# Kernel tuning notes

Measured on AMD Instinct MI355X. Metric: run time of the kernel, lower is better.

Reference implementation:

```python
import jax, jax.numpy as jnp
import numpy as np

EPS_BN = 1e-5
K_INTERP = 8
K_NEIGH = 16


def _bn(x, g, b):
    # BatchNorm1d in training mode: batch stats over rows (biased var), eps=1e-5
    m = x.mean(axis=0)
    v = x.var(axis=0)
    return (x - m) * jax.lax.rsqrt(v + EPS_BN) * g + b


def _dist(a, b):
    # a:(B,N,3), b:(B,M,3) -> Euclidean distance (B,N,M), computed via the
    # quadratic expansion (clamped at 0) instead of materializing (B,N,M,3)
    d2 = (jnp.sum(a * a, -1)[:, :, None] + jnp.sum(b * b, -1)[:, None, :]
          - 2.0 * jnp.einsum('bnc,bmc->bnm', a, b))
    return jnp.sqrt(jnp.maximum(d2, 0.0))


def _gather(feats, idx):
    # feats:(B,M,C), idx:(B,N,K) int -> (B,N,K,C)
    return jax.vmap(lambda f, i: f[i])(feats, idx)


def setup_inputs() -> dict:
    key = jax.random.key(0)
    B, N1, N2, DS, DD, DOUT = 4, 4096, 1024, 128, 64, 256
    ks = jax.random.split(key, 20)
    s = 0.02
    inp = {
        'p1': jax.random.uniform(ks[0], (B * N1, 3), jnp.float32),
        'x1': jax.random.normal(ks[1], (B * N1, DD), jnp.float32),
        'o1': (jnp.arange(B, dtype=jnp.int32) + 1) * N1,
        'p2': jax.random.uniform(ks[2], (B * N2, 3), jnp.float32),
        'x2': jax.random.normal(ks[3], (B * N2, DS), jnp.float32),
        'o2': (jnp.arange(B, dtype=jnp.int32) + 1) * N2,
        'batch_size': B,
        # dense_mlp: Linear(DD,DS) + BN
        'W_dense': jax.random.normal(ks[4], (DD, DS), jnp.float32) * s,
        'b_dense': jnp.zeros((DS,), jnp.float32),
        'g_dense': jnp.ones((DS,), jnp.float32),
        'bt_dense': jnp.zeros((DS,), jnp.float32),
        # CrossAttentionPointTransformerLayer (dim=DS, hidden_mult=1)
        'Wq': jax.random.normal(ks[5], (DS, DS), jnp.float32) * s,
        'Wk': jax.random.normal(ks[6], (DS, DS), jnp.float32) * s,
        'Wv': jax.random.normal(ks[7], (DS, DS), jnp.float32) * s,
        'W1': jax.random.normal(ks[8], (DS, DS), jnp.float32) * s,
        'b1': jnp.zeros((DS,), jnp.float32),
        'g1': jnp.ones((DS,), jnp.float32),
        'bt1': jnp.zeros((DS,), jnp.float32),
        'W2': jax.random.normal(ks[9], (DS, DS), jnp.float32) * s,
        'b2': jnp.zeros((DS,), jnp.float32),
        # output mlp: Linear(DS+DD, DOUT) + BN
        'W_out': jax.random.normal(ks[10], (DS + DD, DOUT), jnp.float32) * s,
        'b_out': jnp.zeros((DOUT,), jnp.float32),
        'g_out': jnp.ones((DOUT,), jnp.float32),
        'bt_out': jnp.zeros((DOUT,), jnp.float32),
    }
    return inp


def reference(p1, x1, o1, p2, x2, o2, batch_size,
              W_dense, b_dense, g_dense, bt_dense,
              Wq, Wk, Wv, W1, b1, g1, bt1, W2, b2,
              W_out, b_out, g_out, bt_out):
    B = int(batch_size)
    N1 = p1.shape[0] // B
    N2 = p2.shape[0] // B
    DS = x2.shape[-1]

    # dense_mlp
    x1_dense = jax.nn.relu(_bn(x1 @ W_dense + b_dense, g_dense, bt_dense))  # (B*N1, DS)

    # pointops.interpolation(p2, p1, x2, o2, o1, k=8): inverse-distance kNN interp
    p1b = p1.reshape(B, N1, 3)
    p2b = p2.reshape(B, N2, 3)
    x2b = x2.reshape(B, N2, DS)
    d12 = _dist(p1b, p2b)                       # (B,N1,N2)
    negd, idx = jax.lax.top_k(-d12, K_INTERP)   # k nearest in p2
    dknn = -negd
    recip = 1.0 / (dknn + 1e-8)
    w = recip / recip.sum(-1, keepdims=True)    # (B,N1,8)
    x2_interp = jnp.einsum('bnk,bnkc->bnc', w, _gather(x2b, idx))  # (B,N1,DS)

    # CrossAttentionPointTransformerLayer(x_e=x1_dense, x_r=x_d=x2_interp, pos=p1)
    x_e = x1_dense.reshape(B, N1, DS)
    q = x_e @ Wq
    k = x2_interp @ Wk
    v = x2_interp @ Wv
    rel_dist = _dist(p1b, p1b)                  # (B,N1,N1)
    _, nidx = jax.lax.top_k(-rel_dist, K_NEIGH) # 16 nearest neighbors
    kg = _gather(k, nidx)                        # (B,N1,16,DS)
    vg = _gather(v, nidx)
    xeg = _gather(x_e, nidx)
    qk_rel = q[:, :, None, :] - kg
    v2 = vg + xeg
    h = (qk_rel + xeg).reshape(-1, DS)           # (B*N1*16, DS)
    h = jax.nn.relu(_bn(h @ W1 + b1, g1, bt1))
    sim = (h @ W2 + b2).reshape(B, N1, K_NEIGH, DS)
    attn = jax.nn.softmax(sim, axis=-2)          # over neighbors
    agg = jnp.einsum('bnkc,bnkc->bnc', attn, v2).reshape(B * N1, DS)

    # output mlp
    x = jax.nn.relu(_bn(jnp.concatenate([agg, x1], axis=-1) @ W_out + b_out,
                        g_out, bt_out))
    return (p1, x, o1)
```

## Files before the change

### kernel.cpp

```cpp
#include <hip/hip_runtime.h>
#include <math.h>

#define BB 4
#define NN1 4096
#define NN2 1024
#define DS 128
#define DD 64
#define DOUT 256
#define M1 16384
#define MH 262144
#define KCAT 192
#define KI 8
#define KN 16

#define OUT_P1 49152
#define OUT_X  49152
#define OUT_O1 4243456


static const size_t OFF_HPRE = 0;
static const size_t OFF_WTS  = 16777216;
static const size_t OFF_TMP  = 33554432;
static const size_t OFF_XD   = OFF_TMP  + 2097152;
static const size_t OFF_XI   = OFF_XD   + 2097152;
static const size_t OFF_Q    = OFF_XI   + 2097152;
static const size_t OFF_K    = OFF_Q    + 2097152;
static const size_t OFF_V    = OFF_K    + 2097152;
static const size_t OFF_OUTP = OFF_V    + 2097152;
static const size_t OFF_NIDX = OFF_OUTP + 4194304;
static const size_t OFF_STAT = OFF_NIDX + 262144;
static const size_t OFF_P1Q  = OFF_STAT + 4096;
static const size_t OFF_P2Q  = OFF_P1Q  + 65536;
static const size_t OFF_P1S  = OFF_P2Q  + 16384;
static const size_t OFF_P2S  = OFF_P1S  + 65536;

#define WDH 0
#define WDL 8192
#define WQH 16384
#define WQL 32768
#define WKH 49152
#define WKL 65536
#define WVH 81920
#define WVL 98304
#define W1H 114688
#define W1L 131072
#define W2H 147456
#define W2L 163840
#define WOH 180224
#define WOL 229376

typedef __attribute__((ext_vector_type(8))) short short8;
typedef __attribute__((ext_vector_type(4))) float floatx4;
typedef __attribute__((ext_vector_type(2))) float float2v;

__device__ inline unsigned short f2bf(float f) {
    union { float f; unsigned int u; } x; x.f = f;
    unsigned int r = x.u + 0x7fffu + ((x.u >> 16) & 1u);
    return (unsigned short)(r >> 16);
}
__device__ inline float bf2f(unsigned short h) {
    union { unsigned int u; float f; } x; x.u = ((unsigned int)h) << 16;
    return x.f;
}
__device__ inline unsigned long long shfl_xor_u64(unsigned long long v, int m) {
    unsigned lo = (unsigned)v, hi = (unsigned)(v >> 32);
    lo = (unsigned)__shfl_xor((int)lo, m);
    hi = (unsigned)__shfl_xor((int)hi, m);
    return ((unsigned long long)hi << 32) | lo;
}

#define PRO_STAT  (OUT_P1 + BB)
#define PRO_PACK  (PRO_STAT + 3072)
#define PRO_TOTAL (PRO_PACK + M1 + BB*NN2)
#define NPRO 285
struct SwzParams {
    const float* W[7];
    unsigned short* hi[7];
    unsigned short* lo[7];
    int N[7];
    int fid0[8];
};
__global__ __launch_bounds__(256) void k_prolog(
    const float* __restrict__ p1, const int* __restrict__ o1,
    const float* __restrict__ p2, float* __restrict__ out,
    float* __restrict__ stat, float4* __restrict__ p1q,
    float4* __restrict__ p2q, float* __restrict__ p1s,
    float* __restrict__ p2s, SwzParams p)
{
    if (blockIdx.x < NPRO) {
        int i = blockIdx.x * 256 + threadIdx.x;
        if (i < OUT_P1) out[i] = p1[i];
        else if (i < PRO_STAT) out[OUT_O1 + (i - OUT_P1)] = (float)o1[i - OUT_P1];
        else if (i < PRO_PACK) stat[i - PRO_STAT] = 0.f;
        else if (i < PRO_TOTAL) {
            int j = i - PRO_PACK;
            const float* src; float4* dst; float* ps; int jj;
            if (j < M1) { src = p1; dst = p1q; ps = p1s; jj = j; }
            else        { src = p2; dst = p2q; ps = p2s; jj = j - M1; }
            float x = src[jj*3+0] * 16384.f;
            float y = src[jj*3+1] * 16384.f;
            float z = src[jj*3+2] * 16384.f;
            float n = fmaf(z, z, fmaf(y, y, x*x));
            dst[jj] = make_float4(x, y, z, n);
            int pb8 = (jj >> 1)*8 + (jj & 1);
            ps[pb8]   = x; ps[pb8+2] = y;
            ps[pb8+4] = z; ps[pb8+6] = n;
        }
        return;
    }
    int fid = (blockIdx.x - NPRO)*4 + (threadIdx.x >> 6);
    int lane = threadIdx.x & 63;
    if (fid >= 272) return;
    int seg = 0;
    #pragma unroll
    for (int i = 1; i < 7; i++) if (fid >= p.fid0[i]) seg = i;
    int f = fid - p.fid0[seg];
    const float* W = p.W[seg];
    int N = p.N[seg];
    int ncj = N >> 4;
    int slab = f / ncj, cj = f - slab*ncj;
    int n  = cj*16 + (lane & 15);
    int k0 = slab*32 + (lane >> 4)*8;
    unsigned int oh[8], ol[8];
    #pragma unroll
    for (int j = 0; j < 8; j++) {
        float v = W[(size_t)(k0 + j) * N + n];
        unsigned short h = f2bf(v);
        oh[j] = h;
        ol[j] = f2bf(v - bf2f(h));
    }
    uint4 ph, pl;
    ph.x = oh[0] | (oh[1] << 16); ph.y = oh[2] | (oh[3] << 16);
    ph.z = oh[4] | (oh[5] << 16); ph.w = oh[6] | (oh[7] << 16);
    pl.x = ol[0] | (ol[1] << 16); pl.y = ol[2] | (ol[3] << 16);
    pl.z = ol[4] | (ol[5] << 16); pl.w = ol[6] | (ol[7] << 16);
    ((uint4*)p.hi[seg])[f*64 + lane] = ph;
    ((uint4*)p.lo[seg])[f*64 + lane] = pl;
}

template<int N, int K, int MODE, int STATS, int BNA>
__global__ __launch_bounds__(256) void k_gemm_mf(
    const float* __restrict__ Amat, const unsigned short* __restrict__ Whi,
    const unsigned short* __restrict__ Wlo, const float* __restrict__ bias,
    float* __restrict__ C, const float* __restrict__ aux,
    float* __restrict__ sums, float* __restrict__ sumsq,
    const float* __restrict__ bsums, const float* __restrict__ bsumsq,
    const float* __restrict__ bg, const float* __restrict__ bbt)
{
    __shared__ float sstat[STATS ? 2*N : 1];
    __shared__ float sbn[BNA ? 2*DS : 1];
    const int t = threadIdx.x, w = t >> 6, lane = t & 63;
    const int quad = lane >> 4, c = lane & 15;
    const int row = blockIdx.x*64 + w*16 + c;
    const int sA = (MODE == 2) ? DS : K;
    constexpr int nslab = K >> 5;
    constexpr int ncj = N >> 4;
    const int seg = (MODE == 3) ? blockIdx.y : 0;
    const float* Abase = (MODE == 3 && seg > 0) ? aux : Amat;
    const unsigned short* WhiS = Whi + (size_t)seg*32768;
    const unsigned short* WloS = Wlo + (size_t)seg*32768;
    float* CS = C + (size_t)seg*2097152;
    unsigned short* CS16 = (unsigned short*)C + (size_t)seg*4194304;
    if (STATS) {
        for (int i = t; i < 2*N; i += 256) sstat[i] = 0.f;
    }
    if (BNA) {
        if (t < DS) {
            const float invM = 1.f / (float)M1;
            float m   = bsums[t] * invM;
            float var = bsumsq[t] * invM - m*m;
            float sc  = bg[t] * rsqrtf(var + 1e-5f);
            sbn[t] = sc;
            sbn[DS + t] = bbt[t] - m * sc;
        }
    }
    if (STATS || BNA) __syncthreads();

    floatx4 acc[ncj];
    #pragma unroll
    for (int cj = 0; cj < ncj; cj++) acc[cj] = (floatx4){0.f,0.f,0.f,0.f};

    #pragma unroll
    for (int slab = 0; slab < nslab; slab++) {
        const int kk = slab*32 + quad*8;
        const float* src;
        if (MODE == 2 && kk >= DS) src = aux + (size_t)row*DD + (kk - DS);
        else                       src = Abase + (size_t)row*sA + kk;
        floatx4 va = *(const floatx4*)src;
        floatx4 vb = *(const floatx4*)(src + 4);
        if (BNA && MODE == 3 && seg == 0) {
            #pragma unroll
            for (int j = 0; j < 4; j++) {
                va[j] = fmaxf(fmaf(va[j], sbn[kk+j],   sbn[DS+kk+j]),   0.f);
                vb[j] = fmaxf(fmaf(vb[j], sbn[kk+4+j], sbn[DS+kk+4+j]), 0.f);
            }
        }
        short8 ahi, alo;
        #pragma unroll
        for (int j = 0; j < 4; j++) {
            unsigned short h = f2bf(va[j]);
            ahi[j] = (short)h; alo[j] = (short)f2bf(va[j] - bf2f(h));
        }
        #pragma unroll
        for (int j = 0; j < 4; j++) {
            unsigned short h = f2bf(vb[j]);
            ahi[4+j] = (short)h; alo[4+j] = (short)f2bf(vb[j] - bf2f(h));
        }
        const short8* bh = (const short8*)WhiS + (size_t)slab*ncj*64;
        const short8* bl = (const short8*)WloS + (size_t)slab*ncj*64;
        #pragma unroll
        for (int cj = 0; cj < ncj; cj++) {
            short8 bhv = bh[cj*64 + lane];
            short8 blv = bl[cj*64 + lane];
            acc[cj] = __builtin_amdgcn_mfma_f32_16x16x32_bf16(alo, bhv, acc[cj], 0, 0, 0);
            acc[cj] = __builtin_amdgcn_mfma_f32_16x16x32_bf16(ahi, blv, acc[cj], 0, 0, 0);
            acc[cj] = __builtin_amdgcn_mfma_f32_16x16x32_bf16(ahi, bhv, acc[cj], 0, 0, 0);
        }
    }
    const int rbase = blockIdx.x*64 + w*16 + quad*4;
    #pragma unroll
    for (int cj = 0; cj < ncj; cj++) {
        const float bb = bias ? bias[cj*16 + c] : 0.f;
        float s = 0.f, ss = 0.f;
        #pragma unroll
        for (int p = 0; p < 4; p++) {
            float v = acc[cj][p] + bb;
            if (MODE == 3) {
                if (seg > 0) {
                    float xv = Amat[(size_t)(rbase + p)*DS + cj*16 + c];
                    if (BNA) xv = fmaxf(fmaf(xv, sbn[cj*16+c], sbn[DS+cj*16+c]), 0.f);
                    if (seg == 1) v = xv - v;
                    else          v += xv;
                }
                CS16[(size_t)(rbase + p)*N + cj*16 + c] = f2bf(v);
            } else {
                CS[(size_t)(rbase + p)*N + cj*16 + c] = v;
            }
            if (STATS) { s += v; ss += v*v; }
        }
        if (STATS) {
            s  += __shfl_xor(s, 16);  s  += __shfl_xor(s, 32);
            ss += __shfl_xor(ss, 16); ss += __shfl_xor(ss, 32);
            if (quad == 0) {
                atomicAdd(&sstat[cj*16 + c], s);
                atomicAdd(&sstat[N + cj*16 + c], ss);
            }
        }
    }
    if (STATS) {
        __syncthreads();
        for (int i = t; i < N; i += 256) {
            atomicAdd(&sums[i],  sstat[i]);
            atomicAdd(&sumsq[i], sstat[N + i]);
        }
    }
}

__global__ __launch_bounds__(256) void k_gemm_h(
    const unsigned short* __restrict__ q, const unsigned short* __restrict__ e,
    const int* __restrict__ nidx,
    const unsigned short* __restrict__ W1sw, const float* __restrict__ b1,
    unsigned short* __restrict__ hpre,
    float* __restrict__ sums, float* __restrict__ sumsq)
{
    __shared__ unsigned short WF[16384];
    __shared__ unsigned short outT[128*128];
    __shared__ float sstat[256];
    const int t = threadIdx.x;
    const int w = t >> 6, lane = t & 63;
    sstat[t] = 0.f;
    #pragma unroll
    for (int i = 0; i < 8; i++)
        ((uint4*)WF)[t + 256*i] = ((const uint4*)W1sw)[t + 256*i];
    __syncthreads();

    const int quad = lane >> 4, c = lane & 15;
    const int r0 = blockIdx.x * 128 + w * 32;
    const int nid0 = nidx[r0 + c];
    const int nid1 = nidx[r0 + 16 + c];
    const int pr0 = r0 >> 4;
    const int pr1 = pr0 + 1;

    floatx4 acc[2][8];
    #pragma unroll
    for (int ti = 0; ti < 2; ti++)
        #pragma unroll
        for (int cj = 0; cj < 8; cj++)
            acc[ti][cj] = (floatx4){0.f, 0.f, 0.f, 0.f};

    for (int ks = 0; ks < 4; ks++) {
        short8 bf[8];
        #pragma unroll
        for (int cj = 0; cj < 8; cj++)
            bf[cj] = ((const short8*)WF)[(ks*8 + cj)*64 + lane];
        const int ko = ks*32 + quad*8;
        #pragma unroll
        for (int ti = 0; ti < 2; ti++) {
            const int pr = ti ? pr1 : pr0;
            const int m  = ti ? nid1 : nid0;
            uint4 qv = *(const uint4*)(q + (size_t)pr*DS + ko);
            uint4 ev = *(const uint4*)(e + (size_t)m*DS + ko);
            unsigned qw[4] = {qv.x, qv.y, qv.z, qv.w};
            unsigned ew[4] = {ev.x, ev.y, ev.z, ev.w};
            short8 af;
            #pragma unroll
            for (int j = 0; j < 4; j++) {
                float f0 = bf2f((unsigned short)(qw[j] & 0xffffu))
                         + bf2f((unsigned short)(ew[j] & 0xffffu));
                float f1 = bf2f((unsigned short)(qw[j] >> 16))
                         + bf2f((unsigned short)(ew[j] >> 16));
                af[2*j]   = (short)f2bf(f0);
                af[2*j+1] = (short)f2bf(f1);
            }
            #pragma unroll
            for (int cj = 0; cj < 8; cj++)
                acc[ti][cj] = __builtin_amdgcn_mfma_f32_16x16x32_bf16(af, bf[cj], acc[ti][cj], 0, 0, 0);
        }
    }

    #pragma unroll
    for (int cj = 0; cj < 8; cj++) {
        const float bb = b1[cj*16 + c];
        float s = 0.f, ss = 0.f;
        #pragma unroll
        for (int ti = 0; ti < 2; ti++)
            #pragma unroll
            for (int p = 0; p < 4; p++) {
                float v = acc[ti][cj][p] + bb;
                s += v; ss += v*v;
                int lr = w*32 + ti*16 + quad*4 + p;
                outT[lr*128 + cj*16 + c] = f2bf(v);
            }
        s  += __shfl_xor(s, 16);  s  += __shfl_xor(s, 32);
        ss += __shfl_xor(ss, 16); ss += __shfl_xor(ss, 32);
        if (quad == 0) {
            atomicAdd(&sstat[cj*16 + c], s);
            atomicAdd(&sstat[128 + cj*16 + c], ss);
        }
    }
    __syncthreads();
    unsigned short* gdst = hpre + (size_t)blockIdx.x * 128 * 128;
    #pragma unroll
    for (int i = 0; i < 8; i++)
        ((uint4*)gdst)[t + 256*i] = ((const uint4*)outT)[t + 256*i];
    if (t < 128) atomicAdd(&sums[t], sstat[t]);
    else         atomicAdd(&sumsq[t - 128], sstat[t]);
}

__global__ __launch_bounds__(256) void k_attn2(
    const unsigned short* __restrict__ hpre, const float* __restrict__ sums_h,
    const float* __restrict__ sumsq_h, const float* __restrict__ g1,
    const float* __restrict__ bt1, const unsigned short* __restrict__ W2sw,
    const unsigned short* __restrict__ v, const int* __restrict__ nidx,
    float* __restrict__ agg)
{
    __shared__ unsigned short WF[16384];
    __shared__ float s_sc[DS], s_sh[DS];
    const int t = threadIdx.x;
    #pragma unroll
    for (int i = 0; i < 8; i++)
        ((uint4*)WF)[t + 256*i] = ((const uint4*)W2sw)[t + 256*i];
    if (t < DS) {
        const float invM = 1.f / (float)MH;
        float m   = sums_h[t] * invM;
        float var = sumsq_h[t] * invM - m*m;
        float sc  = g1[t] * rsqrtf(var + 1e-5f);
        s_sc[t] = sc;
        s_sh[t] = bt1[t] - m * sc;
    }
    __syncthreads();

    const int w = t >> 6, lane = t & 63;
    const int gp = blockIdx.x * 4 + w;
    const int quad = lane >> 4, c = lane & 15;

    floatx4 acc[8];
    #pragma unroll
    for (int cj = 0; cj < 8; cj++) acc[cj] = (floatx4){0.f, 0.f, 0.f, 0.f};

    for (int ks = 0; ks < 4; ks++) {
        const int ko = ks*32 + quad*8;
        const unsigned short* hp = hpre + ((size_t)gp*16 + c)*DS + ko;
        uint4 hv = *(const uint4*)hp;
        floatx4 sc0 = *(const floatx4*)&s_sc[ko];
        floatx4 sc1 = *(const floatx4*)&s_sc[ko + 4];
        floatx4 sh0 = *(const floatx4*)&s_sh[ko];
        floatx4 sh1 = *(const floatx4*)&s_sh[ko + 4];
        unsigned int hw[4] = {hv.x, hv.y, hv.z, hv.w};
        short8 af;
        #pragma unroll
        for (int j = 0; j < 4; j++) {
            unsigned short u0 = (unsigned short)(hw[j] & 0xffffu);
            unsigned short u1 = (unsigned short)(hw[j] >> 16);
            float f0 = fmaxf(fmaf(bf2f(u0), (j<2)?sc0[2*j]:sc1[2*j-4],   (j<2)?sh0[2*j]:sh1[2*j-4]),   0.f);
            float f1 = fmaxf(fmaf(bf2f(u1), (j<2)?sc0[2*j+1]:sc1[2*j-3], (j<2)?sh0[2*j+1]:sh1[2*j-3]), 0.f);
            af[2*j]   = (short)f2bf(f0);
            af[2*j+1] = (short)f2bf(f1);
        }
        #pragma unroll
        for (int cj = 0; cj < 8; cj++) {
            short8 bfv = ((const short8*)WF)[(ks*8 + cj)*64 + lane];
            acc[cj] = __builtin_amdgcn_mfma_f32_16x16x32_bf16(af, bfv, acc[cj], 0, 0, 0);
        }
    }

    int nid[4];
    #pragma unroll
    for (int p = 0; p < 4; p++) nid[p] = nidx[gp*16 + quad*4 + p];

    #pragma unroll
    for (int cj = 0; cj < 8; cj++) {
        float m4 = fmaxf(fmaxf(acc[cj][0], acc[cj][1]), fmaxf(acc[cj][2], acc[cj][3]));
        m4 = fmaxf(m4, __shfl_xor(m4, 16));
        m4 = fmaxf(m4, __shfl_xor(m4, 32));
        float e[4]; float s4 = 0.f;
        #pragma unroll
        for (int p = 0; p < 4; p++) { e[p] = __expf(acc[cj][p] - m4); s4 += e[p]; }
        s4 += __shfl_xor(s4, 16); s4 += __shfl_xor(s4, 32);
        const float inv = 1.f / s4;
        const int col = cj*16 + c;
        float a = 0.f;
        #pragma unroll
        for (int p = 0; p < 4; p++)
            a = fmaf(e[p]*inv, bf2f(v[(size_t)nid[p]*DS + col]), a);
        a += __shfl_xor(a, 16); a += __shfl_xor(a, 32);
        if (quad == 0) agg[(size_t)gp*DS + col] = a;
    }
}

__global__ __launch_bounds__(256) void k_bnrelu(
    const float4* __restrict__ X, const float* __restrict__ sums,
    const float* __restrict__ sumsq, const float* __restrict__ g,
    const float* __restrict__ bt, float invM,
    float4* __restrict__ Y, size_t total4, int N)
{
    size_t i = (size_t)blockIdx.x * 256 + threadIdx.x;
    if (i < total4) {
        int c = (int)((i*4) & (size_t)(N - 1));
        float4 sm = *(const float4*)(sums + c);
        float4 sq = *(const float4*)(sumsq + c);
        float4 gg = *(const float4*)(g + c);
        float4 bb = *(const float4*)(bt + c);
        float4 x = X[i], y;
        float m0 = sm.x*invM, m1 = sm.y*invM, m2 = sm.z*invM, m3 = sm.w*invM;
        float s0 = gg.x*rsqrtf(sq.x*invM - m0*m0 + 1e-5f);
        float s1 = gg.y*rsqrtf(sq.y*invM - m1*m1 + 1e-5f);
        float s2 = gg.z*rsqrtf(sq.z*invM - m2*m2 + 1e-5f);
        float s3 = gg.w*rsqrtf(sq.w*invM - m3*m3 + 1e-5f);
        y.x = fmaxf(fmaf(x.x, s0, bb.x - m0*s0), 0.f);
        y.y = fmaxf(fmaf(x.y, s1, bb.y - m1*s1), 0.f);
        y.z = fmaxf(fmaf(x.z, s2, bb.z - m2*s2), 0.f);
        y.w = fmaxf(fmaf(x.w, s3, bb.w - m3*s3), 0.f);
        Y[i] = y;
    }
}

template<int NCAND, int KSEL, int EPI, int CAP>
__device__ __forceinline__ void sel_body(
    int gp0,
    const float4* __restrict__ qpts4, const float4* __restrict__ cpts4,
    const float* __restrict__ cpairs,
    int* __restrict__ nidx, const float* __restrict__ x2, float* __restrict__ xi,
    unsigned* hist0, unsigned* hist1,
    unsigned* skey, unsigned* sidx,
    float* swtE, unsigned* sidxE,
    unsigned* wpart, int* sstate)
{
    const int b = gp0 >> 12;
    const int t = threadIdx.x, wv = t >> 6, lane = t & 63;
    constexpr int ITER  = NCAND / 256;
    constexpr int PITER = NCAND / 512;

    const float4 qv0 = qpts4[gp0];
    const float4 qv1 = qpts4[gp0 + 1];
    const float4* pb = cpts4 + (size_t)b*NCAND;
    const float*  pbs = cpairs + (size_t)b*NCAND*4;

    unsigned kreg[2][ITER];
    if (t < 16)      ((uint4*)hist0)[t]      = (uint4){0u,0u,0u,0u};
    else if (t < 32) ((uint4*)hist1)[t - 16] = (uint4){0u,0u,0u,0u};
    __syncthreads();

    {
        const float2v qx0 = {qv0.x, qv0.x}, qy0 = {qv0.y, qv0.y};
        const float2v qz0 = {qv0.z, qv0.z}, qw0 = {qv0.w, qv0.w};
        const float2v qx1 = {qv1.x, qv1.x}, qy1 = {qv1.y, qv1.y};
        const float2v qz1 = {qv1.z, qv1.z}, qw1 = {qv1.w, qv1.w};
        const float2v m2 = {-2.f, -2.f}, z2 = {0.f, 0.f};
        #pragma unroll
        for (int pi = 0; pi < PITER; pi++) {
            const int ip = t + 256*pi;
            float4 A  = ((const float4*)pbs)[2*ip];
            float4 Bv = ((const float4*)pbs)[2*ip + 1];
            float2v xp = {A.x, A.y},  yp = {A.z, A.w};
            float2v zp = {Bv.x, Bv.y}, wp = {Bv.z, Bv.w};
            float2v t0 = __builtin_elementwise_fma(yp, qy0, xp*qx0);
            t0 = __builtin_elementwise_fma(zp, qz0, t0);
            float2v d0 = __builtin_elementwise_fma(t0, m2, wp + qw0);
            d0 = __builtin_elementwise_max(d0, z2);
            float2v t1 = __builtin_elementwise_fma(yp, qy1, xp*qx1);
            t1 = __builtin_elementwise_fma(zp, qz1, t1);
            float2v d1 = __builtin_elementwise_fma(t1, m2, wp + qw1);
            d1 = __builtin_elementwise_max(d1, z2);
            unsigned ka = (unsigned)d0[0], kb = (unsigned)d0[1];
            unsigned kc = (unsigned)d1[0], kd = (unsigned)d1[1];
            kreg[0][2*pi] = ka; kreg[0][2*pi+1] = kb;
            kreg[1][2*pi] = kc; kreg[1][2*pi+1] = kd;
            if ((ka >> 20) < CAP) atomicAdd(&hist0[ka >> 20], 1u);
            if ((kb >> 20) < CAP) atomicAdd(&hist0[kb >> 20], 1u);
            if ((kc >> 20) < CAP) atomicAdd(&hist1[kc >> 20], 1u);
            if ((kd >> 20) < CAP) atomicAdd(&hist1[kd >> 20], 1u);
        }
    }
    __syncthreads();

    if (wv < 2) {
        unsigned* H = wv ? hist1 : hist0;
        unsigned h = (lane < CAP) ? H[lane] : 0u;
        unsigned incl = h;
        #pragma unroll
        for (int off = 1; off < 64; off <<= 1) {
            unsigned o = (unsigned)__shfl_up((int)incl, off);
            if (lane >= off) incl += o;
        }
        unsigned excl = incl - h;
        const int base = wv*8;
        if ((int)excl < KSEL && KSEL <= (int)(excl + h)) {
            sstate[base+0] = lane; sstate[base+1] = (int)excl; sstate[base+2] = (int)h;
            sstate[base+3] = ((int)(excl + h) <= 64) ? 1 : 0;
            sstate[base+4] = 0;
        }
        unsigned tot = (unsigned)__shfl((int)incl, 63);
        if (lane == 0 && (int)tot < KSEL) sstate[base+3] = -1;
    }
    __syncthreads();

    if (sstate[3] == -1 || sstate[11] == -1) {
        for (int qi = 0; qi < 2; qi++) {
            if (sstate[qi*8+3] != -1) continue;
            ((uint4*)hist0)[t] = (uint4){0u,0u,0u,0u};
            __syncthreads();
            #pragma unroll
            for (int it = 0; it < ITER; it++)
                atomicAdd(&hist0[kreg[qi][it] >> 20], 1u);
            __syncthreads();
            uint4 h4 = ((const uint4*)hist0)[t];
            unsigned hv[4] = {h4.x, h4.y, h4.z, h4.w};
            unsigned tsum = hv[0]+hv[1]+hv[2]+hv[3];
            unsigned incl = tsum;
            #pragma unroll
            for (int off = 1; off < 64; off <<= 1) {
                unsigned o = (unsigned)__shfl_up((int)incl, off);
                if (lane >= off) incl += o;
            }
            if (lane == 63) wpart[wv] = incl;
            __syncthreads();
            unsigned wbase = 0;
            for (int i2 = 0; i2 < wv; i2++) wbase += wpart[i2];
            unsigned excl = wbase + incl - tsum;
            if ((int)excl < KSEL && KSEL <= (int)(excl + tsum)) {
                unsigned cum = excl;
                #pragma unroll
                for (int i2 = 0; i2 < 4; i2++) {
                    unsigned h = hv[i2];
                    if ((int)cum < KSEL && KSEL <= (int)(cum + h)) {
                        sstate[qi*8+0] = t*4 + i2; sstate[qi*8+1] = (int)cum;
                        sstate[qi*8+2] = (int)h;
                        sstate[qi*8+3] = ((int)cum + (int)h <= 64) ? 1 : 0;
                        sstate[qi*8+4] = 0;
                        break;
                    }
                    cum += h;
                }
            }
            __syncthreads();
        }
    }

    if (sstate[3] == 1 && sstate[11] == 1) {
        const unsigned P0 = (unsigned)sstate[0];
        const unsigned P1 = (unsigned)sstate[8];
        #pragma unroll
        for (int pi = 0; pi < PITER; pi++) {
            const int ip = t + 256*pi;
            #pragma unroll
            for (int c2 = 0; c2 < 2; c2++) {
                const int j = 2*ip + c2;
                const unsigned k0 = kreg[0][2*pi+c2], k1 = kreg[1][2*pi+c2];
                if ((k0 >> 20) <= P0) {
                    int pos = (int)atomicAdd((unsigned*)&sstate[4], 1u);
                    skey[pos] = k0; sidx[pos] = (unsigned)j;
                }
                if ((k1 >> 20) <= P1) {
                    int pos = (int)atomicAdd((unsigned*)&sstate[12], 1u);
                    skey[64 + pos] = k1; sidx[64 + pos] = (unsigned)j;
                }
            }
        }
    } else {
        #pragma unroll
        for (int qi = 0; qi < 2; qi++) {
            const float4 qv = qi ? qv1 : qv0;
            unsigned P = (unsigned)sstate[qi*8+0];
            int S = sstate[qi*8+1], cntB = sstate[qi*8+2], mode = sstate[qi*8+3];
            int gsh = 20;
            if (mode == 0) {
                for (int round = 1; round < 4; round++) {
                    const int nb  = (round == 3) ? 16 : 256;
                    const int wb  = (round == 3) ? 4 : 8;
                    const int sh  = (round == 1) ? 12 : (round == 2 ? 4 : 0);
                    const int psh = sh + wb;
                    if (t < nb) hist0[t] = 0u;
                    __syncthreads();
                    #pragma unroll
                    for (int it = 0; it < ITER; it++) {
                        unsigned key = kreg[qi][it];
                        if ((key >> psh) == P)
                            atomicAdd(&hist0[(key >> sh) & (nb - 1)], 1u);
                    }
                    __syncthreads();
                    unsigned hv = (t < nb) ? hist0[t] : 0u;
                    unsigned tsum = hv;
                    unsigned incl = tsum;
                    #pragma unroll
                    for (int off = 1; off < 64; off <<= 1) {
                        unsigned o = (unsigned)__shfl_up((int)incl, off);
                        if (lane >= off) incl += o;
                    }
                    if (lane == 63) wpart[wv] = incl;
                    __syncthreads();
                    unsigned wbase = 0;
                    for (int i2 = 0; i2 < wv; i2++) wbase += wpart[i2];
                    unsigned exclT = wbase + incl - tsum;
                    const int need = KSEL - S;
                    if ((int)exclT < need && need <= (int)(exclT + tsum)) {
                        int Snew = S + (int)exclT;
                        int tot  = Snew + (int)tsum;
                        sstate[qi*8+0] = (int)((P << wb) | (unsigned)t);
                        sstate[qi*8+1] = Snew; sstate[qi*8+2] = (int)tsum;
                        sstate[qi*8+3] = (tot <= 64) ? 1 : ((round == 3) ? 2 : 0);
                        sstate[qi*8+4] = 0;
                    }
                    __syncthreads();
                    P = (unsigned)sstate[qi*8+0]; S = sstate[qi*8+1];
                    cntB = sstate[qi*8+2]; mode = sstate[qi*8+3];
                    gsh = sh;
                    if (mode) break;
                }
            }
            if (mode == 1) {
                #pragma unroll
                for (int pi = 0; pi < PITER; pi++) {
                    const int ip = t + 256*pi;
                    #pragma unroll
                    for (int c2 = 0; c2 < 2; c2++) {
                        const int j = 2*ip + c2;
                        unsigned key = kreg[qi][2*pi+c2];
                        if ((key >> gsh) <= P) {
                            int pos = (int)atomicAdd((unsigned*)&sstate[qi*8+4], 1u);
                            skey[qi*64 + pos] = key; sidx[qi*64 + pos] = (unsigned)j;
                        }
                    }
                }
            } else if (mode != 1) {
                if (t < 64) {
                    const unsigned long long lmask = (1ull << lane) - 1ull;
                    int cnt = 0;
                    for (int pass = 0; pass < 2; pass++) {
                        for (int it = 0; it < NCAND/64; it++) {
                            int j = lane + 64*it;
                            float4 cv = pb[j];
                            float dot = fmaf(qv.z, cv.z, fmaf(qv.y, cv.y, qv.x*cv.x));
                            float d2 = fmaxf(fmaf(-2.f, dot, qv.w + cv.w), 0.f);
                            unsigned key = (unsigned)d2;
                            bool f = pass ? (key == P) : (key < P);
                            unsigned long long bal = __ballot(f);
                            if (f) {
                                int pos = cnt + __popcll(bal & lmask);
                                if (pos < 64) { skey[qi*64 + pos] = key; sidx[qi*64 + pos] = (unsigned)j; }
                            }
                            cnt += __popcll(bal);
                        }
                    }
                    if (lane == 0) { sstate[qi*8+1] = min(cnt, 64); sstate[qi*8+2] = 0; }
                }
            }
            __syncthreads();
        }
    }
    __syncthreads();

    if (wv < 2) {
        const int q = wv;
        const int total = sstate[q*8+1] + sstate[q*8+2];
        unsigned long long v = ~0ull;
        if (lane < total)
            v = (((unsigned long long)skey[q*64 + lane]) << 32) | sidx[q*64 + lane];
        #pragma unroll
        for (int k = 2; k <= 64; k <<= 1) {
            #pragma unroll
            for (int jj = k >> 1; jj > 0; jj >>= 1) {
                unsigned long long p = shfl_xor_u64(v, jj);
                bool up = ((lane & k) == 0);
                bool takeMin = (((lane & jj) == 0) == up);
                bool pl = p < v;
                v = (takeMin == pl) ? p : v;
            }
        }
        if (EPI == 0) {
            if (lane < KSEL)
                nidx[(gp0 + q)*KSEL + lane] = b*NCAND + (int)(v & 0xffffffffull);
        } else {
            const float4 qq = q ? qv1 : qv0;
            float wgt = 0.f;
            unsigned si = (unsigned)(v & 0xffffffffull);
            if (lane < KSEL) {
                float4 cv = pb[si];
                float dot = fmaf(qq.z, cv.z, fmaf(qq.y, cv.y, qq.x*cv.x));
                float d2 = fmaxf(fmaf(-2.f, dot, qq.w + cv.w), 0.f);
                wgt = 1.f / (sqrtf(d2) + 1.6384e-4f);
            }
            float ws = wgt;
            ws += __shfl_xor(ws, 1); ws += __shfl_xor(ws, 2); ws += __shfl_xor(ws, 4);
            if (lane < KSEL) {
                swtE[q*KSEL + lane]  = wgt / ws;
                sidxE[q*KSEL + lane] = si;
            }
        }
    }

    if (EPI == 1) {
        __syncthreads();
        const int qi2 = t >> 7, tt = t & 127;
        const float* x2b = x2 + (size_t)b*NCAND*DS;
        float a = 0.f;
        #pragma unroll
        for (int r = 0; r < KSEL; r++)
            a = fmaf(swtE[qi2*KSEL + r], x2b[(size_t)sidxE[qi2*KSEL + r]*DS + tt], a);
        xi[(size_t)(gp0 + qi2)*DS + tt] = a;
    }
}

__global__ __launch_bounds__(256) void k_sel2(
    const float4* __restrict__ p1q, const float4* __restrict__ p2q,
    const float* __restrict__ p1s, const float* __restrict__ p2s,
    int* __restrict__ nidx, const float* __restrict__ x2, float* __restrict__ xi)
{
    __shared__ __align__(16) unsigned hist0[1024], hist1[1024];
    __shared__ __align__(16) unsigned skey[128], sidx[128];
    __shared__ float    swtE[2*KI];
    __shared__ unsigned sidxE[2*KI];
    __shared__ unsigned wpart[8];
    __shared__ int      sstate[20];
    const int bid = blockIdx.x;
    if (bid < M1/2) {
        sel_body<NN1, KN, 0, 32>(bid*2, p1q, p1q, p1s, nidx, nullptr, nullptr,
                                 hist0, hist1, skey, sidx, swtE, sidxE, wpart, sstate);
    } else {
        sel_body<NN2, KI, 1, 64>((bid - M1/2)*2, p1q, p2q, p2s, nullptr, x2, xi,
                                 hist0, hist1, skey, sidx, swtE, sidxE, wpart, sstate);
    }
}

extern "C" void kernel_launch(void* const* d_in, const int* in_sizes, int n_in,
                              void* d_out, int out_size, void* d_ws, size_t ws_size,
                              hipStream_t stream)
{
    const float* p1 = (const float*)d_in[0];
    const float* x1 = (const float*)d_in[1];
    const int*   o1 = (const int*)d_in[2];
    const float* p2 = (const float*)d_in[3];
    const float* x2 = (const float*)d_in[4];
    const float* W_dense = (const float*)d_in[7];
    const float* b_dense = (const float*)d_in[8];
    const float* g_dense = (const float*)d_in[9];
    const float* bt_dense= (const float*)d_in[10];
    const float* Wq = (const float*)d_in[11];
    const float* Wk = (const float*)d_in[12];
    const float* Wv = (const float*)d_in[13];
    const float* W1 = (const float*)d_in[14];
    const float* b1 = (const float*)d_in[15];
    const float* g1 = (const float*)d_in[16];
    const float* bt1= (const float*)d_in[17];
    const float* W2 = (const float*)d_in[18];
    const float* W_out = (const float*)d_in[20];
    const float* b_out = (const float*)d_in[21];
    const float* g_out = (const float*)d_in[22];
    const float* bt_out= (const float*)d_in[23];

    float* ws   = (float*)d_ws;
    unsigned short* hpre = (unsigned short*)(ws + OFF_HPRE);
    unsigned short* wts  = (unsigned short*)(ws + OFF_WTS);
    float* tmp  = ws + OFF_TMP;
    float* xi   = ws + OFF_XI;
    float* qm   = ws + OFF_Q;
    float* outp = ws + OFF_OUTP;
    int*   nidx = (int*)(ws + OFF_NIDX);
    float* stat = ws + OFF_STAT;
    float4* p1q = (float4*)(ws + OFF_P1Q);
    float4* p2q = (float4*)(ws + OFF_P2Q);
    float* p1s = ws + OFF_P1S;
    float* p2s = ws + OFF_P2S;
    unsigned short* q16 = (unsigned short*)(ws + OFF_Q);
    unsigned short* e16 = (unsigned short*)(ws + OFF_K);
    unsigned short* v16 = (unsigned short*)(ws + OFF_V);
    float* sums_d = stat,      *sumsq_d = stat+256;
    float* sums_h = stat+1024, *sumsq_h = stat+1280;
    float* sums_o = stat+2048, *sumsq_o = stat+2304;
    float* out = (float*)d_out;

    SwzParams sp;
    sp.W[0]=W_dense; sp.W[1]=Wq; sp.W[2]=Wk; sp.W[3]=Wv; sp.W[4]=W1; sp.W[5]=W2; sp.W[6]=W_out;
    sp.hi[0]=wts+WDH; sp.hi[1]=wts+WQH; sp.hi[2]=wts+WKH; sp.hi[3]=wts+WVH;
    sp.hi[4]=wts+W1H; sp.hi[5]=wts+W2H; sp.hi[6]=wts+WOH;
    sp.lo[0]=wts+WDL; sp.lo[1]=wts+WQL; sp.lo[2]=wts+WKL; sp.lo[3]=wts+WVL;
    sp.lo[4]=wts+W1L; sp.lo[5]=wts+W2L; sp.lo[6]=wts+WOL;
    sp.N[0]=128; sp.N[1]=128; sp.N[2]=128; sp.N[3]=128; sp.N[4]=128; sp.N[5]=128; sp.N[6]=256;
    sp.fid0[0]=0; sp.fid0[1]=16; sp.fid0[2]=48; sp.fid0[3]=80; sp.fid0[4]=112;
    sp.fid0[5]=144; sp.fid0[6]=176; sp.fid0[7]=272;
    k_prolog<<<NPRO + 68, 256, 0, stream>>>(p1, o1, p2, out, stat, p1q, p2q, p1s, p2s, sp);

    k_sel2<<<M1, 256, 0, stream>>>(p1q, p2q, p1s, p2s, nidx, x2, xi);

    k_gemm_mf<128,64,0,1,0><<<M1/64, 256, 0, stream>>>(x1, wts+WDH, wts+WDL, b_dense, tmp,
        nullptr, sums_d, sumsq_d, nullptr, nullptr, nullptr, nullptr);

    k_gemm_mf<128,128,3,0,1><<<dim3(M1/64,3), 256, 0, stream>>>(tmp, wts+WQH, wts+WQL,
        nullptr, qm, xi, nullptr, nullptr, sums_d, sumsq_d, g_dense, bt_dense);

    k_gemm_h<<<MH/128, 256, 0, stream>>>(q16, e16, nidx, wts+W1H, b1, hpre, sums_h, sumsq_h);

    k_attn2<<<M1/4, 256, 0, stream>>>(hpre, sums_h, sumsq_h, g1, bt1, wts+W2H, v16, nidx, tmp);

    k_gemm_mf<256,192,2,1,0><<<M1/64, 256, 0, stream>>>(tmp, wts+WOH, wts+WOL, b_out, outp,
        x1, sums_o, sumsq_o, nullptr, nullptr, nullptr, nullptr);
    k_bnrelu<<<(M1*DOUT/4)/256, 256, 0, stream>>>((const float4*)outp, sums_o, sumsq_o,
        g_out, bt_out, 1.f/(float)M1, (float4*)(out + OUT_X), (size_t)M1*DOUT/4, DOUT);
}
```

Baseline: 336.3 us.

## Distribute W1 over q and gathered e to shrink the hidden GEMM

Instead of running the W1 GEMM on every (point, neighbor) row, it computes q@W1 and e@W1 once per point (16384 rows each) and builds the pre-activation by gathering and adding them in a separate elementwise kernel, which also collects the batch-norm statistics. This cuts MFMA work on the 262144-row hidden GEMM by about 16x, at the cost of writing and re-reading fp32 intermediates and one extra launch. It also drops the bf16 rounding of q+e before the matmul, so numerics change slightly.

```diff
diff --git a/kernel.cpp b/kernel.cpp
--- a/kernel.cpp
+++ b/kernel.cpp
@@ -67,6 +67,11 @@
     lo = (unsigned)__shfl_xor((int)lo, m);
     hi = (unsigned)__shfl_xor((int)hi, m);
     return ((unsigned long long)hi << 32) | lo;
+}
+__device__ inline unsigned cvt_pk_bf16(float lo, float hi) {
+    unsigned r;
+    asm volatile("v_cvt_pk_bf16_f32 %0, %1, %2" : "=v"(r) : "v"(lo), "v"(hi));
+    return r;
 }
 
 #define PRO_STAT  (OUT_P1 + BB)
@@ -256,93 +261,101 @@
     }
 }
 
-__global__ __launch_bounds__(256) void k_gemm_h(
-    const unsigned short* __restrict__ q, const unsigned short* __restrict__ e,
-    const int* __restrict__ nidx,
-    const unsigned short* __restrict__ W1sw, const float* __restrict__ b1,
-    unsigned short* __restrict__ hpre,
+__global__ __launch_bounds__(256) void k_gemm_qe(
+    const unsigned short* __restrict__ q16, const unsigned short* __restrict__ e16,
+    const unsigned short* __restrict__ W1hi, const float* __restrict__ b1,
+    float* __restrict__ qw, float* __restrict__ ew)
+{
+    const int t = threadIdx.x, w = t >> 6, lane = t & 63;
+    const int quad = lane >> 4, c = lane & 15;
+    const int y = blockIdx.y;
+    const unsigned short* A = y ? e16 : q16;
+    float* C = y ? ew : qw;
+    const int row = blockIdx.x*64 + w*16 + c;
+
+    floatx4 acc[8];
+    #pragma unroll
+    for (int cj = 0; cj < 8; cj++) acc[cj] = (floatx4){0.f,0.f,0.f,0.f};
+
+    #pragma unroll
+    for (int slab = 0; slab < 4; slab++) {
+        uint4 av = *(const uint4*)(A + (size_t)row*DS + slab*32 + quad*8);
+        short8 af;
+        ((uint4*)&af)[0] = av;
+        const short8* bh = (const short8*)W1hi + (size_t)slab*8*64;
+        #pragma unroll
+        for (int cj = 0; cj < 8; cj++) {
+            short8 bhv = bh[cj*64 + lane];
+            acc[cj] = __builtin_amdgcn_mfma_f32_16x16x32_bf16(af, bhv, acc[cj], 0, 0, 0);
+        }
+    }
+    const int rbase = blockIdx.x*64 + w*16 + quad*4;
+    #pragma unroll
+    for (int cj = 0; cj < 8; cj++) {
+        const float bb = y ? b1[cj*16 + c] : 0.f;
+        #pragma unroll
+        for (int p = 0; p < 4; p++)
+            C[(size_t)(rbase + p)*DS + cj*16 + c] = acc[cj][p] + bb;
+    }
+}
+
+__global__ __launch_bounds__(256) void k_hadd(
+    const float* __restrict__ qw, const float* __restrict__ ew,
+    const int* __restrict__ nidx, unsigned short* __restrict__ hpre,
     float* __restrict__ sums, float* __restrict__ sumsq)
 {
-    __shared__ unsigned short WF[16384];
-    __shared__ unsigned short outT[128*128];
     __shared__ float sstat[256];
-    const int t = threadIdx.x;
-    const int w = t >> 6, lane = t & 63;
+    const int t = threadIdx.x, w = t >> 6, lane = t & 63;
     sstat[t] = 0.f;
-    #pragma unroll
-    for (int i = 0; i < 8; i++)
-        ((uint4*)WF)[t + 256*i] = ((const uint4*)W1sw)[t + 256*i];
     __syncthreads();
-
-    const int quad = lane >> 4, c = lane & 15;
-    const int r0 = blockIdx.x * 128 + w * 32;
-    const int nid0 = nidx[r0 + c];
-    const int nid1 = nidx[r0 + 16 + c];
-    const int pr0 = r0 >> 4;
-    const int pr1 = pr0 + 1;
-
-    floatx4 acc[2][8];
-    #pragma unroll
-    for (int ti = 0; ti < 2; ti++)
-        #pragma unroll
-        for (int cj = 0; cj < 8; cj++)
-            acc[ti][cj] = (floatx4){0.f, 0.f, 0.f, 0.f};
-
-    for (int ks = 0; ks < 4; ks++) {
-        short8 bf[8];
-        #pragma unroll
-        for (int cj = 0; cj < 8; cj++)
-            bf[cj] = ((const short8*)WF)[(ks*8 + cj)*64 + lane];
-        const int ko = ks*32 + quad*8;
-        #pragma unroll
-        for (int ti = 0; ti < 2; ti++) {
-            const int pr = ti ? pr1 : pr0;
-            const int m  = ti ? nid1 : nid0;
-            uint4 qv = *(const uint4*)(q + (size_t)pr*DS + ko);
-            uint4 ev = *(const uint4*)(e + (size_t)m*DS + ko);
-            unsigned qw[4] = {qv.x, qv.y, qv.z, qv.w};
-            unsigned ew[4] = {ev.x, ev.y, ev.z, ev.w};
-            short8 af;
-            #pragma unroll
-            for (int j = 0; j < 4; j++) {
-                float f0 = bf2f((unsigned short)(qw[j] & 0xffffu))
-                         + bf2f((unsigned short)(ew[j] & 0xffffu));
-                float f1 = bf2f((unsigned short)(qw[j] >> 16))
-                         + bf2f((unsigned short)(ew[j] >> 16));
-                af[2*j]   = (short)f2bf(f0);
-                af[2*j+1] = (short)f2bf(f1);
-            }
-            #pragma unroll
-            for (int cj = 0; cj < 8; cj++)
-                acc[ti][cj] = __builtin_amdgcn_mfma_f32_16x16x32_bf16(af, bf[cj], acc[ti][cj], 0, 0, 0);
-        }
-    }
-
-    #pragma unroll
-    for (int cj = 0; cj < 8; cj++) {
-        const float bb = b1[cj*16 + c];
-        float s = 0.f, ss = 0.f;
-        #pragma unroll
-        for (int ti = 0; ti < 2; ti++)
-            #pragma unroll
-            for (int p = 0; p < 4; p++) {
-                float v = acc[ti][cj][p] + bb;
-                s += v; ss += v*v;
-                int lr = w*32 + ti*16 + quad*4 + p;
-                outT[lr*128 + cj*16 + c] = f2bf(v);
-            }
-        s  += __shfl_xor(s, 16);  s  += __shfl_xor(s, 32);
-        ss += __shfl_xor(ss, 16); ss += __shfl_xor(ss, 32);
-        if (quad == 0) {
-            atomicAdd(&sstat[cj*16 + c], s);
-            atomicAdd(&sstat[128 + cj*16 + c], ss);
+    const int rr = lane & 7, cg = lane >> 3;
+    const int wr0 = blockIdx.x*128 + w*32;
+    const int cb = cg*16;
+
+    float sv[16], sq[16];
+    #pragma unroll
+    for (int j = 0; j < 16; j++) { sv[j] = 0.f; sq[j] = 0.f; }
+
+    #pragma unroll
+    for (int p = 0; p < 4; p++) {
+        const int r = wr0 + p*8 + rr;
+        const int i = r >> 4;
+        const int m = nidx[r];
+        const float4* Ap = (const float4*)(qw + (size_t)i*DS + cb);
+        const float4* Bp = (const float4*)(ew + (size_t)m*DS + cb);
+        float4 a0 = Ap[0], a1 = Ap[1], a2 = Ap[2], a3 = Ap[3];
+        float4 b0 = Bp[0], b1v = Bp[1], b2 = Bp[2], b3 = Bp[3];
+        float v[16];
+        v[0]=a0.x+b0.x;  v[1]=a0.y+b0.y;  v[2]=a0.z+b0.z;  v[3]=a0.w+b0.w;
+        v[4]=a1.x+b1v.x; v[5]=a1.y+b1v.y; v[6]=a1.z+b1v.z; v[7]=a1.w+b1v.w;
+        v[8]=a2.x+b2.x;  v[9]=a2.y+b2.y;  v[10]=a2.z+b2.z; v[11]=a2.w+b2.w;
+        v[12]=a3.x+b3.x; v[13]=a3.y+b3.y; v[14]=a3.z+b3.z; v[15]=a3.w+b3.w;
+        #pragma unroll
+        for (int j = 0; j < 16; j++) { sv[j] += v[j]; sq[j] = fmaf(v[j], v[j], sq[j]); }
+        uint4 pk0, pk1;
+        pk0.x = cvt_pk_bf16(v[0],  v[1]);  pk0.y = cvt_pk_bf16(v[2],  v[3]);
+        pk0.z = cvt_pk_bf16(v[4],  v[5]);  pk0.w = cvt_pk_bf16(v[6],  v[7]);
+        pk1.x = cvt_pk_bf16(v[8],  v[9]);  pk1.y = cvt_pk_bf16(v[10], v[11]);
+        pk1.z = cvt_pk_bf16(v[12], v[13]); pk1.w = cvt_pk_bf16(v[14], v[15]);
+        uint4* dst = (uint4*)(hpre + (size_t)r*DS + cb);
+        dst[0] = pk0; dst[1] = pk1;
+    }
+    #pragma unroll
+    for (int m2 = 1; m2 < 8; m2 <<= 1) {
+        #pragma unroll
+        for (int j = 0; j < 16; j++) {
+            sv[j] += __shfl_xor(sv[j], m2);
+            sq[j] += __shfl_xor(sq[j], m2);
+        }
+    }
+    if (rr == 0) {
+        #pragma unroll
+        for (int j = 0; j < 16; j++) {
+            atomicAdd(&sstat[cb + j], sv[j]);
+            atomicAdd(&sstat[128 + cb + j], sq[j]);
         }
     }
     __syncthreads();
-    unsigned short* gdst = hpre + (size_t)blockIdx.x * 128 * 128;
-    #pragma unroll
-    for (int i = 0; i < 8; i++)
-        ((uint4*)gdst)[t + 256*i] = ((const uint4*)outT)[t + 256*i];
     if (t < 128) atomicAdd(&sums[t], sstat[t]);
     else         atomicAdd(&sumsq[t - 128], sstat[t]);
 }
@@ -792,6 +805,8 @@
     unsigned short* hpre = (unsigned short*)(ws + OFF_HPRE);
     unsigned short* wts  = (unsigned short*)(ws + OFF_WTS);
     float* tmp  = ws + OFF_TMP;
+    float* qw1f = ws + OFF_XD;
+    float* ew1f = ws + OFF_OUTP;
     float* xi   = ws + OFF_XI;
     float* qm   = ws + OFF_Q;
     float* outp = ws + OFF_OUTP;
@@ -828,7 +843,8 @@
     k_gemm_mf<128,128,3,0,1><<<dim3(M1/64,3), 256, 0, stream>>>(tmp, wts+WQH, wts+WQL,
         nullptr, qm, xi, nullptr, nullptr, sums_d, sumsq_d, g_dense, bt_dense);
 
-    k_gemm_h<<<MH/128, 256, 0, stream>>>(q16, e16, nidx, wts+W1H, b1, hpre, sums_h, sumsq_h);
+    k_gemm_qe<<<dim3(M1/64, 2), 256, 0, stream>>>(q16, e16, wts+W1H, b1, qw1f, ew1f);
+    k_hadd<<<MH/128, 256, 0, stream>>>(qw1f, ew1f, nidx, hpre, sums_h, sumsq_h);
 
     k_attn2<<<M1/4, 256, 0, stream>>>(hpre, sums_h, sumsq_h, g1, bt1, wts+W2H, v16, nidx, tmp);
 
```

Result: no change. 342.3 us (+1.8%).
